# Kernel optimization log

Hardware: AMD Instinct MI355X
Metric: run time of the kernel (lower is better)

Reference implementation:

```python
import jax, jax.numpy as jnp
import numpy as np

TEMPERATURE = 0.0005

def conv1d(x, w, b):
    # x: [B,Cin,T], w: [Cout,Cin,K], 'same' padding as ConvNorm (pad=(K-1)//2)
    pad = (w.shape[-1] - 1) // 2
    y = jax.lax.conv_general_dilated(x, w, window_strides=(1,), padding=[(pad, pad)],
                                     dimension_numbers=('NCH', 'OIH', 'NCH'))
    return y + b[None, :, None]

def setup_inputs() -> dict:
    key = jax.random.key(0)
    ks = jax.random.split(key, 20)
    B, C_MEL, C_TXT, C_ATT, T1, T2 = 32, 80, 512, 80, 1600, 400
    s = 0.02
    return {
        'queries': jax.random.normal(ks[0], (B, C_MEL, T1), jnp.float32),
        'keys': jax.random.normal(ks[1], (B, C_TXT, T2), jnp.float32),
        'mask': jax.random.randint(ks[2], (B, T2, 1), 0, 2).astype(bool),
        'attn_prior': jax.random.uniform(ks[3], (B, T1, T2), jnp.float32),
        'speaker_embed': jax.random.normal(ks[4], (B, C_TXT), jnp.float32),
        # key_proj: Conv(512->1024,k3) -> ReLU -> Conv(1024->80,k1)
        'Wk1': jax.random.normal(ks[5], (C_TXT * 2, C_TXT, 3)) * s,
        'bk1': jax.random.normal(ks[6], (C_TXT * 2,)) * s,
        'Wk2': jax.random.normal(ks[7], (C_ATT, C_TXT * 2, 1)) * s,
        'bk2': jax.random.normal(ks[8], (C_ATT,)) * s,
        # query_proj: Conv(80->160,k3) -> ReLU -> Conv(160->80,k1) -> ReLU -> Conv(80->80,k1)
        'Wq1': jax.random.normal(ks[9], (C_MEL * 2, C_MEL, 3)) * s,
        'bq1': jax.random.normal(ks[10], (C_MEL * 2,)) * s,
        'Wq2': jax.random.normal(ks[11], (C_MEL, C_MEL * 2, 1)) * s,
        'bq2': jax.random.normal(ks[12], (C_MEL,)) * s,
        'Wq3': jax.random.normal(ks[13], (C_ATT, C_MEL, 1)) * s,
        'bq3': jax.random.normal(ks[14], (C_ATT,)) * s,
        # speaker projections (multi_speaker=True)
        'Wks': jax.random.normal(ks[15], (C_TXT, C_TXT)) * s,
        'bks': jax.random.normal(ks[16], (C_TXT,)) * s,
        'Wqs': jax.random.normal(ks[17], (C_MEL, C_TXT)) * s,
        'bqs': jax.random.normal(ks[18], (C_MEL,)) * s,
    }

def reference(queries, keys, mask, attn_prior, speaker_embed,
              Wk1, bk1, Wk2, bk2, Wq1, bq1, Wq2, bq2, Wq3, bq3,
              Wks, bks, Wqs, bqs):
    # speaker conditioning: Linear(spk) broadcast over time, added channelwise
    keys = keys + (speaker_embed @ Wks.T + bks)[:, :, None]
    queries = queries + (speaker_embed @ Wqs.T + bqs)[:, :, None]
    # projections
    k = jax.nn.relu(conv1d(keys, Wk1, bk1))
    k = conv1d(k, Wk2, bk2)                      # [B, C_att, T2]
    q = jax.nn.relu(conv1d(queries, Wq1, bq1))
    q = jax.nn.relu(conv1d(q, Wq2, bq2))
    q = conv1d(q, Wq3, bq3)                      # [B, C_att, T1]
    # -temp * sum_c (q-k)^2 == -temp * (||q||^2 + ||k||^2 - 2 q.k)
    q2 = jnp.sum(q * q, axis=1)                  # [B, T1]
    k2 = jnp.sum(k * k, axis=1)                  # [B, T2]
    qk = jnp.einsum('bct,bcs->bts', q, k)        # [B, T1, T2]
    attn = -TEMPERATURE * (q2[:, :, None] + k2[:, None, :] - 2.0 * qk)
    attn = attn[:, None]                         # [B, 1, T1, T2]
    attn = jax.nn.log_softmax(attn, axis=3) + jnp.log(attn_prior[:, None] + 1e-8)
    attn_logprob = attn
    m = jnp.transpose(mask, (0, 2, 1))[:, :, None, :]  # [B,1,1,T2]
    attn = jnp.where(m, -jnp.inf, attn)
    attn = jax.nn.softmax(attn, axis=3)
    return attn, attn_logprob
```

## Files before the change

### kernel.cpp

```cpp
#include <hip/hip_runtime.h>
#include <math.h>

#define TEMP 0.0005f
#define B_    32
#define CMEL  80
#define CTXT  512
#define T1_   1600
#define T2_   400

typedef short short8 __attribute__((ext_vector_type(8)));
typedef float f32x4 __attribute__((ext_vector_type(4)));

__device__ inline unsigned short f2bf(float f) {
    unsigned u = __float_as_uint(f);
    u += 0x7FFF + ((u >> 16) & 1);
    return (unsigned short)(u >> 16);
}
__device__ inline unsigned pack2(float a, float b) {
    return (unsigned)f2bf(a) | ((unsigned)f2bf(b) << 16);
}

__global__ void bias_kernel(const float* __restrict__ se,
                            const float* __restrict__ Wks, const float* __restrict__ bks,
                            const float* __restrict__ Wqs, const float* __restrict__ bqs,
                            float* __restrict__ kb, float* __restrict__ qb) {
    int tid = blockIdx.x * blockDim.x + threadIdx.x;
    const int nk = B_ * CTXT;
    if (tid < nk) {
        int b = tid / CTXT, c = tid % CTXT;
        const float4* s4 = reinterpret_cast<const float4*>(se + b * CTXT);
        const float4* w4 = reinterpret_cast<const float4*>(Wks + (size_t)c * CTXT);
        float acc = bks[c];
        #pragma unroll 4
        for (int j = 0; j < CTXT / 4; ++j) {
            float4 a = s4[j], w = w4[j];
            acc += a.x * w.x + a.y * w.y + a.z * w.z + a.w * w.w;
        }
        kb[tid] = acc;
    } else if (tid < nk + B_ * CMEL) {
        int t = tid - nk;
        int b = t / CMEL, c = t % CMEL;
        const float4* s4 = reinterpret_cast<const float4*>(se + b * CTXT);
        const float4* w4 = reinterpret_cast<const float4*>(Wqs + (size_t)c * CTXT);
        float acc = bqs[c];
        #pragma unroll 4
        for (int j = 0; j < CTXT / 4; ++j) {
            float4 a = s4[j], w = w4[j];
            acc += a.x * w.x + a.y * w.y + a.z * w.z + a.w * w.w;
        }
        qb[t] = acc;
    }
}

__global__ void cast_weights_kernel(
        const float* __restrict__ Wk1, const float* __restrict__ Wk2,
        const float* __restrict__ Wq1, const float* __restrict__ Wq2,
        const float* __restrict__ Wq3,
        unsigned short* __restrict__ Ab1, unsigned short* __restrict__ A2,
        unsigned short* __restrict__ A3, unsigned short* __restrict__ A4,
        unsigned short* __restrict__ A5) {
    int e = blockIdx.x * 256 + threadIdx.x;
    const int n1 = 1572864, n2 = 81920, n3 = 46080, n4 = 12800, n5 = 7680;
    if (e < n1) {
        int co = e / 1536, rem = e - co * 1536;
        int dt = rem >> 9, ci = rem & 511;
        Ab1[e] = f2bf(Wk1[((size_t)co * 512 + ci) * 3 + dt]);
    } else if ((e -= n1) < n2) {
        A2[e] = f2bf(Wk2[e]);
    } else if ((e -= n2) < n3) {
        int co = e / 288, rem = e - co * 288;
        int dt = rem / 96, cc = rem - dt * 96;
        A3[e] = (cc < 80) ? f2bf(Wq1[((size_t)co * 80 + cc) * 3 + dt]) : 0;
    } else if ((e -= n3) < n4) {
        A4[e] = f2bf(Wq2[e]);
    } else if ((e -= n4) < n5) {
        int co = e / 96, cc = e - co * 96;
        A5[e] = (cc < 80) ? f2bf(Wq3[co * 80 + cc]) : 0;
    }
}

__global__ void castXk_kernel(const float* __restrict__ keys, const float* __restrict__ kb,
                              unsigned short* __restrict__ Xt) {
    __shared__ float tile[64][65];
    const int b = blockIdx.z;
    const int row0 = blockIdx.x * 64;
    const int ci0 = blockIdx.y * 64;
    const int tid = threadIdx.x;
    #pragma unroll
    for (int i = 0; i < 16; ++i) {
        int linear = i * 256 + tid;
        int ci_l = linear >> 6, t_l = linear & 63;
        int t = row0 + t_l - 1;
        float v = 0.f;
        if (t >= 0 && t < 400)
            v = keys[((size_t)b * 512 + ci0 + ci_l) * 400 + t] + kb[b * 512 + ci0 + ci_l];
        tile[t_l][ci_l] = v;
    }
    __syncthreads();
    #pragma unroll
    for (int i = 0; i < 16; ++i) {
        int linear = i * 256 + tid;
        int t_l = linear >> 6, ci_l = linear & 63;
        int row = row0 + t_l;
        if (row < 456)
            Xt[((size_t)b * 456 + row) * 512 + ci0 + ci_l] = f2bf(tile[t_l][ci_l]);
    }
}

__global__ __launch_bounds__(256) void castXq_kernel(
        const float* __restrict__ q, const float* __restrict__ qb,
        unsigned short* __restrict__ Xq1) {
    __shared__ float tile[80][65];
    const int b = blockIdx.y;
    const int t0 = blockIdx.x * 64;
    const int tid = threadIdx.x;
    if (t0 == 0 && tid < 48)
        ((unsigned*)(Xq1 + (size_t)b * 1602 * 96))[tid] = 0u;
    if (t0 == 1536 && tid < 48)
        ((unsigned*)(Xq1 + ((size_t)b * 1602 + 1601) * 96))[tid] = 0u;
    {
        int tl = tid & 63, c0 = tid >> 6;
        for (int c = c0; c < 80; c += 4)
            tile[c][tl] = q[((size_t)b * 80 + c) * 1600 + t0 + tl] + qb[b * 80 + c];
    }
    __syncthreads();
    int row = tid >> 2, cg = tid & 3;
    int t = t0 + row;
    unsigned* orow = (unsigned*)(Xq1 + ((size_t)b * 1602 + t + 1) * 96 + cg * 24);
    #pragma unroll
    for (int jj = 0; jj < 12; ++jj) {
        int c0 = cg * 24 + jj * 2, c1 = c0 + 1;
        float f0 = (c0 < 80) ? tile[c0][row] : 0.f;
        float f1 = (c1 < 80) ? tile[c1][row] : 0.f;
        orow[jj] = pack2(f0, f1);
    }
}

__global__ __launch_bounds__(256) void conv1k_mfma(
        const unsigned short* __restrict__ Ab, const unsigned short* __restrict__ Xt,
        const float* __restrict__ bias, unsigned short* __restrict__ k1c) {
    __shared__ short As[3 * 128 * 40];
    __shared__ short Xs[66 * 40];
    const int b = blockIdx.z;
    const int co0 = blockIdx.y * 128;
    const int t0 = blockIdx.x * 64;
    const int tid = threadIdx.x;
    const int lane = tid & 63, w = tid >> 6;
    const int wm = w >> 1, wn = w & 1;
    const int l15 = lane & 15, quad = lane >> 4;
    f32x4 acc[4][2];
    #pragma unroll
    for (int mt = 0; mt < 4; ++mt)
        #pragma unroll
        for (int nt = 0; nt < 2; ++nt)
            acc[mt][nt] = (f32x4){0.f, 0.f, 0.f, 0.f};

    for (int ci0 = 0; ci0 < 512; ci0 += 32) {
        __syncthreads();
        #pragma unroll
        for (int i = 0; i < 6; ++i) {
            int linear = i * 256 + tid;
            int dt = linear >> 9;
            int rem = linear & 511;
            int r = rem >> 2, c16 = rem & 3;
            int4 v = *(const int4*)(Ab + (size_t)(co0 + r) * 1536 + dt * 512 + ci0 + c16 * 8);
            *(int4*)(As + (dt * 128 + r) * 40 + c16 * 8) = v;
        }
        #pragma unroll
        for (int i = 0; i < 2; ++i) {
            int c = i * 256 + tid;
            if (c < 264) {
                int row = c >> 2, c16 = c & 3;
                int4 v = *(const int4*)(Xt + ((size_t)b * 456 + t0 + row) * 512 + ci0 + c16 * 8);
                *(int4*)(Xs + row * 40 + c16 * 8) = v;
            }
        }
        __syncthreads();
        #pragma unroll
        for (int dt = 0; dt < 3; ++dt) {
            short8 af[4], bfr[2];
            #pragma unroll
            for (int mt = 0; mt < 4; ++mt)
                af[mt] = *(const short8*)(As + (dt * 128 + wm * 64 + mt * 16 + l15) * 40 + quad * 8);
            #pragma unroll
            for (int nt = 0; nt < 2; ++nt)
                bfr[nt] = *(const short8*)(Xs + (wn * 32 + nt * 16 + l15 + dt) * 40 + quad * 8);
            #pragma unroll
            for (int mt = 0; mt < 4; ++mt)
                #pragma unroll
                for (int nt = 0; nt < 2; ++nt)
                    acc[mt][nt] = __builtin_amdgcn_mfma_f32_16x16x32_bf16(af[mt], bfr[nt], acc[mt][nt], 0, 0, 0);
        }
    }
    #pragma unroll
    for (int mt = 0; mt < 4; ++mt) {
        int cob = co0 + wm * 64 + mt * 16 + quad * 4;
        float bv[4];
        #pragma unroll
        for (int r = 0; r < 4; ++r) bv[r] = bias[cob + r];
        #pragma unroll
        for (int nt = 0; nt < 2; ++nt) {
            int t = t0 + wn * 32 + nt * 16 + l15;
            if (t >= 400) continue;
            float v0 = fmaxf(acc[mt][nt][0] + bv[0], 0.f);
            float v1 = fmaxf(acc[mt][nt][1] + bv[1], 0.f);
            float v2 = fmaxf(acc[mt][nt][2] + bv[2], 0.f);
            float v3 = fmaxf(acc[mt][nt][3] + bv[3], 0.f);
            uint2 p;
            p.x = pack2(v0, v1);
            p.y = pack2(v2, v3);
            *(uint2*)(k1c + ((size_t)b * 400 + t) * 1024 + cob) = p;
        }
    }
}

template<int MT, int NKC, int DTC, bool RELU, int OMODE, int INW, int OUTW, int N, int NR>
__global__ __launch_bounds__(256) void gemm_cl(
        const unsigned short* __restrict__ A, const unsigned short* __restrict__ X,
        const float* __restrict__ bias, unsigned short* __restrict__ out) {
    const int b = blockIdx.y;
    const int tid = threadIdx.x;
    const int lane = tid & 63, w = tid >> 6;
    const int l15 = lane & 15, quad = lane >> 4;
    const int s = blockIdx.x * 64 + w * 16 + l15;
    const int srow = (s < N) ? s : (N - 1);
    const unsigned short* xb = X + (size_t)b * NR * INW;

    f32x4 acc[MT];
    #pragma unroll
    for (int mt = 0; mt < MT; ++mt) acc[mt] = (f32x4){0.f, 0.f, 0.f, 0.f};

    #pragma unroll
    for (int kc = 0; kc < NKC; ++kc) {
        const int dt = DTC ? (kc / DTC) : 0;
        const int koff = DTC ? ((kc - dt * DTC) * 32) : (kc * 32);
        short8 bfr = *(const short8*)(xb + (size_t)(srow + dt) * INW + koff + quad * 8);
        #pragma unroll
        for (int mt = 0; mt < MT; ++mt) {
            short8 af = *(const short8*)(A + (size_t)(mt * 16 + l15) * (NKC * 32) + kc * 32 + quad * 8);
            acc[mt] = __builtin_amdgcn_mfma_f32_16x16x32_bf16(af, bfr, acc[mt], 0, 0, 0);
        }
    }
    if (s >= N) return;

    float v[MT][4];
    float ss = 0.f;
    #pragma unroll
    for (int mt = 0; mt < MT; ++mt) {
        #pragma unroll
        for (int r = 0; r < 4; ++r) {
            float x = acc[mt][r] + bias[mt * 16 + quad * 4 + r];
            if (RELU) x = fmaxf(x, 0.f);
            v[mt][r] = x;
            if (OMODE >= 2) ss += x * x;
        }
    }
    if (OMODE >= 2) {
        ss += __shfl_xor(ss, 16, 64);
        ss += __shfl_xor(ss, 32, 64);
    }
    unsigned short* orow = out + ((size_t)b * N + s) * OUTW;
    #pragma unroll
    for (int mt = 0; mt < MT; ++mt) {
        uint2 p;
        p.x = pack2(v[mt][0], v[mt][1]);
        p.y = pack2(v[mt][2], v[mt][3]);
        *(uint2*)(orow + mt * 16 + quad * 4) = p;
    }
    if (OMODE == 1 && quad == 0) {
        uint4 z = {0u, 0u, 0u, 0u};
        *(uint4*)(orow + 80) = z;
        *(uint4*)(orow + 88) = z;
    }
    if (OMODE >= 2 && quad == 0) {
        float e80 = (OMODE == 2) ? (-0.5f * ss) : 1.0f;
        float e81 = (OMODE == 2) ? 1.0f : (-0.5f * ss);
        uint4 z0 = {pack2(e80, e81), 0u, 0u, 0u};
        uint4 z1 = {0u, 0u, 0u, 0u};
        *(uint4*)(orow + 80) = z0;
        *(uint4*)(orow + 88) = z1;
    }
}

__global__ __launch_bounds__(256) void attn_mfma_kernel(
        const unsigned short* __restrict__ qT, const unsigned short* __restrict__ kT,
        const int* __restrict__ mask, const float* __restrict__ prior,
        float* __restrict__ attn_out, float* __restrict__ lp_out) {
    __shared__ float msh[400];
    const int b = blockIdx.y;
    const int t10 = blockIdx.x * 64;
    const int tid = threadIdx.x;
    const int lane = tid & 63, w = tid >> 6;
    const int l15 = lane & 15, quad = lane >> 4;
    for (int s = tid; s < 400; s += 256)
        msh[s] = mask[b * T2_ + s] ? 1.f : 0.f;
    __syncthreads();

    const unsigned short* qrow = qT + ((size_t)b * T1_ + t10 + w * 16 + l15) * 96;
    short8 af[3];
    #pragma unroll
    for (int kc = 0; kc < 3; ++kc)
        af[kc] = *(const short8*)(qrow + kc * 32 + quad * 8);

    f32x4 acc[25];
    #pragma unroll
    for (int ns = 0; ns < 25; ++ns) acc[ns] = (f32x4){0.f, 0.f, 0.f, 0.f};
    const unsigned short* kbase = kT + (size_t)b * T2_ * 96 + l15 * 96 + quad * 8;
    #pragma unroll
    for (int ns = 0; ns < 25; ++ns) {
        #pragma unroll
        for (int kc = 0; kc < 3; ++kc) {
            short8 bf = *(const short8*)(kbase + ns * 16 * 96 + kc * 32);
            acc[ns] = __builtin_amdgcn_mfma_f32_16x16x32_bf16(af[kc], bf, acc[ns], 0, 0, 0);
        }
    }

    const float NEG = -INFINITY;
    const float K2T = 2.0f * TEMP;
    #pragma unroll
    for (int r = 0; r < 4; ++r) {
        const int t1 = t10 + w * 16 + quad * 4 + r;
        float l[25];
        #pragma unroll
        for (int ns = 0; ns < 25; ++ns) l[ns] = K2T * acc[ns][r];
        float m = l[0];
        #pragma unroll
        for (int ns = 1; ns < 25; ++ns) m = fmaxf(m, l[ns]);
        #pragma unroll
        for (int off = 1; off <= 8; off <<= 1) m = fmaxf(m, __shfl_xor(m, off, 16));
        float sum = 0.f;
        #pragma unroll
        for (int ns = 0; ns < 25; ++ns) sum += __expf(l[ns] - m);
        #pragma unroll
        for (int off = 1; off <= 8; off <<= 1) sum += __shfl_xor(sum, off, 16);
        const float lse = m + __logf(sum);

        const float* prow = prior + ((size_t)b * T1_ + t1) * T2_;
        float* lpr = lp_out + ((size_t)b * T1_ + t1) * T2_;
        float* atr = attn_out + ((size_t)b * T1_ + t1) * T2_;
        #pragma unroll
        for (int ns = 0; ns < 25; ++ns) {
            int s = ns * 16 + l15;
            float lp = l[ns] - lse + __logf(prow[s] + 1e-8f);
            lpr[s] = lp;
            l[ns] = (msh[s] != 0.f) ? NEG : lp;
        }
        float m2 = NEG;
        #pragma unroll
        for (int ns = 0; ns < 25; ++ns) m2 = fmaxf(m2, l[ns]);
        #pragma unroll
        for (int off = 1; off <= 8; off <<= 1) m2 = fmaxf(m2, __shfl_xor(m2, off, 16));
        float s2 = 0.f;
        #pragma unroll
        for (int ns = 0; ns < 25; ++ns) { float e = __expf(l[ns] - m2); s2 += e; l[ns] = e; }
        #pragma unroll
        for (int off = 1; off <= 8; off <<= 1) s2 += __shfl_xor(s2, off, 16);
        const float inv = 1.f / s2;
        #pragma unroll
        for (int ns = 0; ns < 25; ++ns) atr[ns * 16 + l15] = l[ns] * inv;
    }
}

extern "C" void kernel_launch(void* const* d_in, const int* in_sizes, int n_in,
                              void* d_out, int out_size, void* d_ws, size_t ws_size,
                              hipStream_t stream) {
    const float* queries = (const float*)d_in[0];
    const float* keys    = (const float*)d_in[1];
    const int*   mask    = (const int*)d_in[2];
    const float* prior   = (const float*)d_in[3];
    const float* se      = (const float*)d_in[4];
    const float* Wk1 = (const float*)d_in[5];
    const float* bk1 = (const float*)d_in[6];
    const float* Wk2 = (const float*)d_in[7];
    const float* bk2 = (const float*)d_in[8];
    const float* Wq1 = (const float*)d_in[9];
    const float* bq1 = (const float*)d_in[10];
    const float* Wq2 = (const float*)d_in[11];
    const float* bq2 = (const float*)d_in[12];
    const float* Wq3 = (const float*)d_in[13];
    const float* bq3 = (const float*)d_in[14];
    const float* Wks = (const float*)d_in[15];
    const float* bks = (const float*)d_in[16];
    const float* Wqs = (const float*)d_in[17];
    const float* bqs = (const float*)d_in[18];

    float* ws = (float*)d_ws;
    float* kb = ws;
    float* qb = ws + 16384;
    unsigned short* Ab1 = (unsigned short*)(ws + 18944);
    unsigned short* A2  = (unsigned short*)(ws + 805376);
    unsigned short* A3  = (unsigned short*)(ws + 846336);
    unsigned short* A4  = (unsigned short*)(ws + 869376);
    unsigned short* A5  = (unsigned short*)(ws + 875776);
    unsigned short* qT  = (unsigned short*)(ws + 879616);
    unsigned short* kT  = (unsigned short*)(ws + 3337216);
    const size_t D = 3951616;
    unsigned short* Xk  = (unsigned short*)(ws + D);
    unsigned short* k1c = (unsigned short*)(ws + D + 3735552);
    unsigned short* Xq1 = (unsigned short*)(ws + D);
    unsigned short* Xq2 = (unsigned short*)(ws + D + 2460672);
    unsigned short* Xq3 = (unsigned short*)(ws + D);

    float* attn_out = (float*)d_out;
    float* lp_out   = attn_out + (size_t)B_ * T1_ * T2_;

    bias_kernel<<<dim3(74), dim3(256), 0, stream>>>(se, Wks, bks, Wqs, bqs, kb, qb);
    cast_weights_kernel<<<dim3(6724), dim3(256), 0, stream>>>(Wk1, Wk2, Wq1, Wq2, Wq3,
                                                              Ab1, A2, A3, A4, A5);
    castXk_kernel<<<dim3(8, 8, 32), dim3(256), 0, stream>>>(keys, kb, Xk);
    conv1k_mfma<<<dim3(7, 8, 32), dim3(256), 0, stream>>>(Ab1, Xk, bk1, k1c);
    gemm_cl<5, 32, 0, false, 2, 1024, 96, 400, 400>
        <<<dim3(7, 32), 256, 0, stream>>>(A2, k1c, bk2, kT);
    castXq_kernel<<<dim3(25, 32), dim3(256), 0, stream>>>(queries, qb, Xq1);
    gemm_cl<10, 9, 3, true, 0, 96, 160, 1600, 1602>
        <<<dim3(25, 32), 256, 0, stream>>>(A3, Xq1, bq1, Xq2);
    gemm_cl<5, 5, 0, true, 1, 160, 96, 1600, 1600>
        <<<dim3(25, 32), 256, 0, stream>>>(A4, Xq2, bq2, Xq3);
    gemm_cl<5, 3, 0, false, 3, 96, 96, 1600, 1600>
        <<<dim3(25, 32), 256, 0, stream>>>(A5, Xq3, bq3, qT);
    attn_mfma_kernel<<<dim3(25, 32), 256, 0, stream>>>(qT, kT, mask, prior, attn_out, lp_out);
}
```

Baseline: 603.8 us.

## Derive masked softmax from first-softmax exponentials times prior; single-wave attention blocks

The second softmax is computed algebraically as exp(l-m)*(prior+eps)*keep normalized, reusing the first softmax exponentials instead of a second max/exp pass. This drops one max reduction and 25 exps per row. The attention kernel is also changed to one 64-thread wave per block, with mask values held in registers instead of shared memory, which removes the __syncthreads. Prior loads are hoisted ahead of the math. Numerical behavior changes slightly, since the result now relies on the unnormalized exponentials not underflowing and a fully masked row divides by zero.

```diff
diff --git a/kernel.cpp b/kernel.cpp
--- a/kernel.cpp
+++ b/kernel.cpp
@@ -282,21 +282,21 @@
     }
 }
 
-__global__ __launch_bounds__(256) void attn_mfma_kernel(
+__global__ __launch_bounds__(64) void attn_mfma_kernel(
         const unsigned short* __restrict__ qT, const unsigned short* __restrict__ kT,
         const int* __restrict__ mask, const float* __restrict__ prior,
         float* __restrict__ attn_out, float* __restrict__ lp_out) {
-    __shared__ float msh[400];
     const int b = blockIdx.y;
-    const int t10 = blockIdx.x * 64;
-    const int tid = threadIdx.x;
-    const int lane = tid & 63, w = tid >> 6;
+    const int t10 = blockIdx.x * 16;
+    const int lane = threadIdx.x;
     const int l15 = lane & 15, quad = lane >> 4;
-    for (int s = tid; s < 400; s += 256)
-        msh[s] = mask[b * T2_ + s] ? 1.f : 0.f;
-    __syncthreads();
-
-    const unsigned short* qrow = qT + ((size_t)b * T1_ + t10 + w * 16 + l15) * 96;
+
+    float keep[25];
+    #pragma unroll
+    for (int ns = 0; ns < 25; ++ns)
+        keep[ns] = mask[b * T2_ + ns * 16 + l15] ? 0.f : 1.f;
+
+    const unsigned short* qrow = qT + ((size_t)b * T1_ + t10 + l15) * 96;
     short8 af[3];
     #pragma unroll
     for (int kc = 0; kc < 3; ++kc)
@@ -315,11 +315,15 @@
         }
     }
 
-    const float NEG = -INFINITY;
     const float K2T = 2.0f * TEMP;
     #pragma unroll
     for (int r = 0; r < 4; ++r) {
-        const int t1 = t10 + w * 16 + quad * 4 + r;
+        const int t1 = t10 + quad * 4 + r;
+        const float* prow = prior + ((size_t)b * T1_ + t1) * T2_;
+        float pe[25];
+        #pragma unroll
+        for (int ns = 0; ns < 25; ++ns) pe[ns] = prow[ns * 16 + l15] + 1e-8f;
+
         float l[25];
         #pragma unroll
         for (int ns = 0; ns < 25; ++ns) l[ns] = K2T * acc[ns][r];
@@ -328,36 +332,31 @@
         for (int ns = 1; ns < 25; ++ns) m = fmaxf(m, l[ns]);
         #pragma unroll
         for (int off = 1; off <= 8; off <<= 1) m = fmaxf(m, __shfl_xor(m, off, 16));
+        float e1[25];
         float sum = 0.f;
         #pragma unroll
-        for (int ns = 0; ns < 25; ++ns) sum += __expf(l[ns] - m);
+        for (int ns = 0; ns < 25; ++ns) { float e = __expf(l[ns] - m); e1[ns] = e; sum += e; }
         #pragma unroll
         for (int off = 1; off <= 8; off <<= 1) sum += __shfl_xor(sum, off, 16);
         const float lse = m + __logf(sum);
 
-        const float* prow = prior + ((size_t)b * T1_ + t1) * T2_;
         float* lpr = lp_out + ((size_t)b * T1_ + t1) * T2_;
         float* atr = attn_out + ((size_t)b * T1_ + t1) * T2_;
+        float u[25];
+        float sum2 = 0.f;
         #pragma unroll
         for (int ns = 0; ns < 25; ++ns) {
-            int s = ns * 16 + l15;
-            float lp = l[ns] - lse + __logf(prow[s] + 1e-8f);
-            lpr[s] = lp;
-            l[ns] = (msh[s] != 0.f) ? NEG : lp;
-        }
-        float m2 = NEG;
-        #pragma unroll
-        for (int ns = 0; ns < 25; ++ns) m2 = fmaxf(m2, l[ns]);
-        #pragma unroll
-        for (int off = 1; off <= 8; off <<= 1) m2 = fmaxf(m2, __shfl_xor(m2, off, 16));
-        float s2 = 0.f;
-        #pragma unroll
-        for (int ns = 0; ns < 25; ++ns) { float e = __expf(l[ns] - m2); s2 += e; l[ns] = e; }
-        #pragma unroll
-        for (int off = 1; off <= 8; off <<= 1) s2 += __shfl_xor(s2, off, 16);
-        const float inv = 1.f / s2;
-        #pragma unroll
-        for (int ns = 0; ns < 25; ++ns) atr[ns * 16 + l15] = l[ns] * inv;
+            float lp = l[ns] - lse + __logf(pe[ns]);
+            lpr[ns * 16 + l15] = lp;
+            float uu = e1[ns] * pe[ns] * keep[ns];
+            u[ns] = uu;
+            sum2 += uu;
+        }
+        #pragma unroll
+        for (int off = 1; off <= 8; off <<= 1) sum2 += __shfl_xor(sum2, off, 16);
+        const float inv = 1.f / sum2;
+        #pragma unroll
+        for (int ns = 0; ns < 25; ++ns) atr[ns * 16 + l15] = u[ns] * inv;
     }
 }
 
@@ -418,5 +417,5 @@
         <<<dim3(25, 32), 256, 0, stream>>>(A4, Xq2, bq2, Xq3);
     gemm_cl<5, 3, 0, false, 3, 96, 96, 1600, 1600>
         <<<dim3(25, 32), 256, 0, stream>>>(A5, Xq3, bq3, qT);
-    attn_mfma_kernel<<<dim3(25, 32), 256, 0, stream>>>(qT, kT, mask, prior, attn_out, lp_out);
-}
+    attn_mfma_kernel<<<dim3(100, 32), dim3(64), 0, stream>>>(qT, kT, mask, prior, attn_out, lp_out);
+}
```

After: 612.0 us. Within noise of the previous version (+1.3%).
